# Optimization experiments

Hardware: AMD Instinct MI355X
Metric: run time of the kernel (lower is better)

## Reference

```python
import jax, jax.numpy as jnp
from jax import lax
import numpy as np

B, N, M, C, K = 2, 16384, 4096, 16, 32
RADIUS = 0.1
EPS = 1e-8


def setup_inputs() -> dict:
    key = jax.random.key(0)
    ks = jax.random.split(key, 9)
    return {
        "xyz": jax.random.uniform(ks[0], (B, N, 3), jnp.float32),
        "new_xyz": jax.random.uniform(ks[1], (B, M, 3), jnp.float32),
        "features": jax.random.normal(ks[2], (B, C, N), jnp.float32),
        "w0": jax.random.normal(ks[3], (32, C), jnp.float32) * 0.1,
        "b0": jax.random.normal(ks[4], (32,), jnp.float32) * 0.1,
        "w1": jax.random.normal(ks[5], (64, 32), jnp.float32) * 0.1,
        "b1": jax.random.normal(ks[6], (64,), jnp.float32) * 0.1,
        "wxyz": jax.random.normal(ks[7], (32, 3), jnp.float32) * 0.1,
        "bxyz": jax.random.normal(ks[8], (32,), jnp.float32) * 0.1,
    }


def ball_query(xyz, new_xyz, radius, nsample):
    """Return (idx [B,M,K] int32, idn multiplicity [B,M,K] int32, has_any [B,M] bool).
    Matches pointnet2 ball_query: first `nsample` in-radius indices (ascending),
    empty slots padded with the first found index; idn counts how many times an
    index is duplicated in a row (0 everywhere for rows with no neighbor)."""
    d2 = jnp.sum((new_xyz[:, :, None, :] - xyz[:, None, :, :]) ** 2, axis=-1)  # B,M,N
    n = xyz.shape[1]
    score = jnp.where(d2 < radius * radius,
                      jnp.arange(n, dtype=jnp.int32), jnp.int32(n))
    idx = -lax.top_k(-score, nsample)[0]          # B,M,K smallest indices, asc
    valid = idx < n
    idx = jnp.where(valid, idx, idx[..., :1])      # pad with first found index
    has_any = valid[..., 0]
    idx = jnp.where(idx >= n, 0, idx)              # safe gather for empty rows
    cnt = jnp.sum(idx[..., :, None] == idx[..., None, :], axis=-1).astype(jnp.int32)
    idn = jnp.where(has_any[..., None], cnt, 0)
    return idx, idn, has_any


def reference(xyz, new_xyz, features, w0, b0, w1, b1, wxyz, bxyz):
    idx, idn, has_any = ball_query(xyz, new_xyz, RADIUS, K)
    b_idx = jnp.arange(xyz.shape[0])[:, None, None]
    # QueryAndGroup: relative coords + gathered features
    rel = xyz[b_idx, idx] - new_xyz[:, :, None, :]            # B,M,K,3
    rel = jnp.transpose(rel, (0, 3, 1, 2))                    # B,3,M,K
    gfeat = jnp.transpose(features, (0, 2, 1))[b_idx, idx]    # B,M,K,C
    gfeat = jnp.transpose(gfeat, (0, 3, 1, 2))                # B,C,M,K

    # distance-reciprocal weights, duplicate-corrected by idn, row-normalized
    dist = jnp.linalg.norm(rel, axis=1, keepdims=True)        # B,1,M,K
    dist_recip = 1.0 / (dist + EPS)
    _idn = jnp.where(has_any[:, None, :, None], idn[:, None, :, :], 1).astype(dist.dtype)
    dist_recip = dist_recip / _idn
    weights = dist_recip / jnp.sum(dist_recip, axis=3, keepdims=True)
    idn_mask = has_any[:, None, :, None].astype(dist.dtype)
    weights = weights * idn_mask                              # zero empty rows

    # SharedMLP on features: 1x1 conv == per-point matmul, ReLU
    h = jax.nn.relu(jnp.einsum('bcmk,oc->bomk', gfeat, w0) + b0[None, :, None, None])
    h = jax.nn.relu(jnp.einsum('bcmk,oc->bomk', h, w1) + b1[None, :, None, None])
    feat_sum = jnp.sum(weights * h, axis=3)                   # B,64,M weighted sum-pool

    # xyz branch: SharedMLP [3,32] + max-pool over neighbors
    hx = jax.nn.relu(jnp.einsum('bcmk,oc->bomk', rel, wxyz) + bxyz[None, :, None, None])
    feat_max = jnp.max(hx, axis=3)                            # B,32,M

    return new_xyz, jnp.concatenate([feat_max, feat_sum], axis=1)  # (B,M,3),(B,96,M)
```

## Files before the change

kernel.cpp:

```cpp
#include <hip/hip_runtime.h>
#include <math.h>
#include <limits.h>

#define BB 2
#define NN 16384
#define MM 4096
#define CCH 16
#define KK 32
#define R2 0.01f
#define EPSV 1e-8f
#define GD 10
#define CPB (GD*GD*GD)
#define CAP 56
#define NCELL (BB*CPB)
#define BUCKET_OFF 16384
#define FEATT_OFF (2*1024*1024)
#define WS_GRID (BUCKET_OFF + (size_t)NCELL*CAP*16)
#define WS_FT   (FEATT_OFF + (size_t)BB*NN*CCH*4)
#define NDW 512

typedef __attribute__((ext_vector_type(8))) short short8;
typedef __attribute__((ext_vector_type(4))) float v4f;

__device__ __forceinline__ short f2bf(float f) {
    unsigned u = __float_as_uint(f);
    unsigned r = u + 0x7FFFu + ((u >> 16) & 1u);
    return (short)(r >> 16);
}

__device__ __forceinline__ int cell_of(float x, float y, float z) {
    int cx = min(GD-1, max(0, (int)(x * 10.0f)));
    int cy = min(GD-1, max(0, (int)(y * 10.0f)));
    int cz = min(GD-1, max(0, (int)(z * 10.0f)));
    return (cx*GD + cy)*GD + cz;
}

__global__ void k_scatter(const float* __restrict__ xyz, const float* __restrict__ feat,
                          int* __restrict__ cnt, int* __restrict__ ovf,
                          float4* __restrict__ buckets, float4* __restrict__ featT,
                          int use_ft) {
    int i = blockIdx.x*256 + threadIdx.x;
    if (i >= BB*NN) return;
    const float* p = xyz + (size_t)i*3;
    int b = i >> 14;
    int n = i & (NN-1);
    float x = p[0], y = p[1], z = p[2];
    int cell = b*CPB + cell_of(x, y, z);
    int slot = atomicAdd(&cnt[cell], 1);
    if (slot < CAP)
        buckets[(size_t)cell*CAP + slot] = make_float4(x, y, z, __int_as_float(n));
    else
        *ovf = 1;
    if (use_ft) {
        const float* fb = feat + (size_t)b*CCH*NN + n;
        #pragma unroll
        for (int c4 = 0; c4 < 4; ++c4) {
            float4 t = make_float4(fb[(c4*4+0)*NN], fb[(c4*4+1)*NN],
                                   fb[(c4*4+2)*NN], fb[(c4*4+3)*NN]);
            featT[(size_t)i*4 + c4] = t;
        }
    }
}

__global__ __launch_bounds__(256, 4) void grouper_fused(
    const float* __restrict__ xyz, const float* __restrict__ new_xyz,
    const float* __restrict__ feat,
    const float* __restrict__ w0, const float* __restrict__ b0,
    const float* __restrict__ w1, const float* __restrict__ b1,
    const float* __restrict__ wxyz, const float* __restrict__ bxyz,
    const int* __restrict__ cnt, const int* __restrict__ ovf,
    const float4* __restrict__ buckets, const float4* __restrict__ featT,
    int use_grid, int use_ft,
    float* __restrict__ out)
{
    const int lane = threadIdx.x & 63;
    const int wid  = threadIdx.x >> 6;
    const int q    = (blockIdx.x << 2) + wid;
    const int b    = q >> 12;
    const int m    = q & (MM - 1);

    __shared__ int s_idx[4][KK];
    __shared__ float4 s_rel[4][KK];
    __shared__ __align__(16) unsigned s_bm[4][NDW];

    const float* xb = xyz + (size_t)b * NN * 3;
    const float qx = new_xyz[((size_t)b*MM + m)*3 + 0];
    const float qy = new_xyz[((size_t)b*MM + m)*3 + 1];
    const float qz = new_xyz[((size_t)b*MM + m)*3 + 2];
    const unsigned long long below = (1ull << lane) - 1ull;

    int nfound = 0, idx0 = 0;
    bool need_full = (use_grid == 0) || (use_grid && ovf[0] != 0);

    if (!need_full) {
        uint4 z4 = make_uint4(0u, 0u, 0u, 0u);
        *(uint4*)&s_bm[wid][lane*8]     = z4;
        *(uint4*)&s_bm[wid][lane*8 + 4] = z4;

        int x0 = max(0, (int)floorf((qx - 0.1f)*10.0f - 1e-3f));
        int x1 = min(GD-1, (int)floorf((qx + 0.1f)*10.0f + 1e-3f));
        int y0 = max(0, (int)floorf((qy - 0.1f)*10.0f - 1e-3f));
        int y1 = min(GD-1, (int)floorf((qy + 0.1f)*10.0f + 1e-3f));
        int z0 = max(0, (int)floorf((qz - 0.1f)*10.0f - 1e-3f));
        int z1 = min(GD-1, (int)floorf((qz + 0.1f)*10.0f + 1e-3f));

        int myCell = -1, ncells = 0;
        int myCx = 0, myCy = 0, myCz = 0;
        for (int cx = x0; cx <= x1; ++cx)
        for (int cy = y0; cy <= y1; ++cy)
        for (int cz = z0; cz <= z1; ++cz) {
            if (lane == ncells) {
                myCell = b*CPB + (cx*GD + cy)*GD + cz;
                myCx = cx; myCy = cy; myCz = cz;
            }
            ++ncells;
        }
        int myCnt = 0, myBase = 0;
        if (myCell >= 0) {
            float xlo = myCx*0.1f, ylo = myCy*0.1f, zlo = myCz*0.1f;
            float ddx = fmaxf(fmaxf(xlo - qx, qx - (xlo + 0.1f)), 0.0f);
            float ddy = fmaxf(fmaxf(ylo - qy, qy - (ylo + 0.1f)), 0.0f);
            float ddz = fmaxf(fmaxf(zlo - qz, qz - (zlo + 0.1f)), 0.0f);
            if (ddx*ddx + ddy*ddy + ddz*ddz < R2) {
                myCnt = min(cnt[myCell], CAP);
                myBase = myCell*CAP;
            }
        }

        __builtin_amdgcn_wave_barrier();

        int cc0 = __builtin_amdgcn_readlane(myCnt, 0);
        int cb0 = __builtin_amdgcn_readlane(myBase, 0);
        float4 p0 = make_float4(0.f, 0.f, 0.f, 0.f);
        if (lane < cc0) p0 = buckets[cb0 + lane];
        for (int c = 0; c < ncells; ++c) {
            int cc1 = 0, cb1 = 0;
            if (c + 1 < ncells) {
                cc1 = __builtin_amdgcn_readlane(myCnt, c + 1);
                cb1 = __builtin_amdgcn_readlane(myBase, c + 1);
            }
            float4 pn = make_float4(0.f, 0.f, 0.f, 0.f);
            if (lane < cc1) pn = buckets[cb1 + lane];
            if (lane < cc0) {
                float dx = p0.x - qx, dy = p0.y - qy, dz = p0.z - qz;
                float d2 = dx*dx + dy*dy + dz*dz;
                if (d2 < R2) {
                    int id = __float_as_int(p0.w);
                    atomicOr(&s_bm[wid][id >> 5], 1u << (id & 31));
                }
            }
            cc0 = cc1; cb0 = cb1; p0 = pn;
        }

        __builtin_amdgcn_wave_barrier();

        uint4 d0 = *(uint4*)&s_bm[wid][lane*8];
        uint4 d1 = *(uint4*)&s_bm[wid][lane*8 + 4];
        unsigned dw[8] = {d0.x, d0.y, d0.z, d0.w, d1.x, d1.y, d1.z, d1.w};
        int pc = 0;
        #pragma unroll
        for (int j = 0; j < 8; ++j) pc += __popc(dw[j]);
        int pre = pc;
        #pragma unroll
        for (int d = 1; d < 64; d <<= 1) {
            int t = __shfl_up(pre, d);
            if (lane >= d) pre += t;
        }
        int total = __shfl(pre, 63);
        int rank = pre - pc;
        nfound = min(total, KK);

        if (rank < KK) {
            #pragma unroll
            for (int j = 0; j < 8; ++j) {
                unsigned bits = dw[j];
                while (bits && rank < KK) {
                    int bpos = __builtin_ctz(bits);
                    s_idx[wid][rank] = ((lane*8 + j) << 5) + bpos;
                    bits &= bits - 1;
                    ++rank;
                }
            }
        }

        __builtin_amdgcn_wave_barrier();
        idx0 = (nfound > 0) ? s_idx[wid][0] : 0;
        __builtin_amdgcn_wave_barrier();
        if (lane >= nfound && lane < KK) s_idx[wid][lane] = idx0;
        __builtin_amdgcn_wave_barrier();
    }

    if (need_full) {
        int cntf = 0;
        for (int basep = 0; basep < NN; basep += 256) {
            float d2a[4];
            #pragma unroll
            for (int j = 0; j < 4; ++j) {
                int i = basep + (j << 6) + lane;
                float px = xb[i*3+0], py = xb[i*3+1], pz = xb[i*3+2];
                float dx = px - qx, dy = py - qy, dz = pz - qz;
                d2a[j] = dx*dx + dy*dy + dz*dz;
            }
            #pragma unroll
            for (int j = 0; j < 4; ++j) {
                bool hit = d2a[j] < R2;
                unsigned long long msk = __ballot(hit);
                if (hit) {
                    int pos = cntf + __popcll(msk & below);
                    if (pos < KK) s_idx[wid][pos] = basep + (j << 6) + lane;
                }
                cntf += __popcll(msk);
            }
            if (cntf >= KK) break;
        }
        nfound = cntf < KK ? cntf : KK;
        __builtin_amdgcn_wave_barrier();
        if (lane < KK) {
            int v = 0;
            if (nfound > 0) v = (lane < nfound) ? s_idx[wid][lane] : s_idx[wid][0];
            s_idx[wid][lane] = v;
        }
        __builtin_amdgcn_wave_barrier();
        idx0 = s_idx[wid][0];
    }

    {
        const int k = lane & 31;
        const int h = lane >> 5;
        const int ik = s_idx[wid][k];
        float px = xb[ik*3+0], py = xb[ik*3+1], pz = xb[ik*3+2];
        float rx = px - qx, ry = py - qy, rz = pz - qz;
        float dist = sqrtf(rx*rx + ry*ry + rz*rz);
        float recip = 1.0f / (dist + EPSV);
        float mult = (float)(1 + KK - nfound);
        float w = recip / ((ik == idx0) ? mult : 1.0f);
        float S = w;
        #pragma unroll
        for (int d = 1; d < 32; d <<= 1) S += __shfl_xor(S, d);
        float wk = (nfound > 0) ? (w / S) : 0.0f;
        if (h == 0) s_rel[wid][k] = make_float4(rx, ry, rz, wk);
    }
    __builtin_amdgcn_wave_barrier();

    const int l15 = lane & 15;
    const int quad = lane >> 4;
    const int ik0 = s_idx[wid][l15];
    const int ik1 = s_idx[wid][16 + l15];

    float g0[CCH], g1[CCH];
    if (use_ft) {
        const float4* f0 = featT + ((size_t)(b*NN + ik0)) * 4;
        const float4* f1 = featT + ((size_t)(b*NN + ik1)) * 4;
        #pragma unroll
        for (int c4 = 0; c4 < 4; ++c4) {
            float4 a = f0[c4], c = f1[c4];
            g0[c4*4+0] = a.x; g0[c4*4+1] = a.y; g0[c4*4+2] = a.z; g0[c4*4+3] = a.w;
            g1[c4*4+0] = c.x; g1[c4*4+1] = c.y; g1[c4*4+2] = c.z; g1[c4*4+3] = c.w;
        }
    } else {
        const float* fb = feat + (size_t)b * CCH * NN;
        #pragma unroll
        for (int c = 0; c < CCH; ++c) { g0[c] = fb[c*NN + ik0]; g1[c] = fb[c*NN + ik1]; }
    }

    short8 A0, A1;
    #pragma unroll
    for (int j = 0; j < 8; ++j) {
        const int o = (quad << 3) + j;
        const float* wr = w0 + o*CCH;
        float a0 = 0.f, a1 = 0.f;
        #pragma unroll
        for (int c = 0; c < CCH; ++c) { a0 += wr[c]*g0[c]; a1 += wr[c]*g1[c]; }
        float bo = b0[o];
        A0[j] = f2bf(fmaxf(a0 + bo, 0.0f));
        A1[j] = f2bf(fmaxf(a1 + bo, 0.0f));
    }

    short8 Bf[4];
    #pragma unroll
    for (int u = 0; u < 4; ++u) {
        const float* wr = w1 + ((u << 4) + l15)*32 + (quad << 3);
        float4 p = *(const float4*)(wr);
        float4 r = *(const float4*)(wr + 4);
        short8 bb;
        bb[0]=f2bf(p.x); bb[1]=f2bf(p.y); bb[2]=f2bf(p.z); bb[3]=f2bf(p.w);
        bb[4]=f2bf(r.x); bb[5]=f2bf(r.y); bb[6]=f2bf(r.z); bb[7]=f2bf(r.w);
        Bf[u] = bb;
    }

    v4f zero4 = {0.f, 0.f, 0.f, 0.f};
    v4f D[2][4];
    #pragma unroll
    for (int u = 0; u < 4; ++u) {
        D[0][u] = __builtin_amdgcn_mfma_f32_16x16x32_bf16(A0, Bf[u], zero4, 0, 0, 0);
        D[1][u] = __builtin_amdgcn_mfma_f32_16x16x32_bf16(A1, Bf[u], zero4, 0, 0, 0);
    }

    float wkv[2][4];
    #pragma unroll
    for (int t = 0; t < 2; ++t)
        #pragma unroll
        for (int r = 0; r < 4; ++r)
            wkv[t][r] = s_rel[wid][16*t + (quad << 2) + r].w;

    float* out2 = out + (size_t)BB*MM*3 + (size_t)b*96*MM;

    float Su[4];
    #pragma unroll
    for (int u = 0; u < 4; ++u) {
        const float b1O = b1[(u << 4) + l15];
        float s = 0.f;
        #pragma unroll
        for (int t = 0; t < 2; ++t)
            #pragma unroll
            for (int r = 0; r < 4; ++r)
                s += wkv[t][r] * fmaxf(D[t][u][r] + b1O, 0.0f);
        s += __shfl_xor(s, 16);
        s += __shfl_xor(s, 32);
        Su[u] = s;
    }
    float sout = (quad == 0) ? Su[0] : (quad == 1) ? Su[1] : (quad == 2) ? Su[2] : Su[3];
    out2[(32 + lane)*MM + m] = sout;

    {
        const int c = lane & 31;
        const int h = lane >> 5;
        const float wx0 = wxyz[c*3+0], wx1 = wxyz[c*3+1], wx2 = wxyz[c*3+2];
        const float bc = bxyz[c];
        float v = 0.0f;
        #pragma unroll
        for (int kk = 0; kk < 16; ++kk) {
            float4 hr = s_rel[wid][(h << 4) + kk];
            float t = bc + wx0*hr.x + wx1*hr.y + wx2*hr.z;
            v = fmaxf(v, fmaxf(t, 0.0f));
        }
        v = fmaxf(v, __shfl_xor(v, 32));
        if (h == 0) out2[c*MM + m] = v;
    }

    if (lane == 0) {
        float* o0 = out + ((size_t)b*MM + m)*3;
        o0[0] = qx; o0[1] = qy; o0[2] = qz;
    }
}

extern "C" void kernel_launch(void* const* d_in, const int* in_sizes, int n_in,
                              void* d_out, int out_size, void* d_ws, size_t ws_size,
                              hipStream_t stream) {
    const float* xyz     = (const float*)d_in[0];
    const float* new_xyz = (const float*)d_in[1];
    const float* feat    = (const float*)d_in[2];
    const float* w0      = (const float*)d_in[3];
    const float* b0      = (const float*)d_in[4];
    const float* w1      = (const float*)d_in[5];
    const float* b1      = (const float*)d_in[6];
    const float* wxyz    = (const float*)d_in[7];
    const float* bxyz    = (const float*)d_in[8];
    float* out = (float*)d_out;

    int* ovf = (int*)d_ws;
    int* cnt = (int*)((char*)d_ws + 64);
    float4* buckets = (float4*)((char*)d_ws + BUCKET_OFF);
    float4* featT   = (float4*)((char*)d_ws + FEATT_OFF);
    const int use_grid = (d_ws != nullptr && ws_size >= WS_GRID) ? 1 : 0;
    const int use_ft   = (d_ws != nullptr && ws_size >= WS_FT) ? 1 : 0;

    if (use_grid) {
        hipMemsetAsync(d_ws, 0, BUCKET_OFF, stream);
        hipLaunchKernelGGL(k_scatter, dim3((BB*NN+255)/256), dim3(256), 0, stream,
                           xyz, feat, cnt, ovf, buckets, featT, use_ft);
    }
    hipLaunchKernelGGL(grouper_fused, dim3((BB*MM)/4), dim3(256), 0, stream,
                       xyz, new_xyz, feat, w0, b0, w1, b1, wxyz, bxyz,
                       cnt, ovf, buckets, featT, use_grid, use_ft, out);
}
```

Measured before the change: 120.6 us.

## Move first MLP layer onto MFMA and precompute bf16 weight fragments

The first 16->32 layer, previously scalar FMAs per lane, now runs as bf16 MFMA. Its output is staged through shared memory, transposed into the A operand of the second MFMA, and the biases are folded into the accumulators. The scatter kernel no longer builds a transposed feature copy; instead it converts w0 and w1 once into bf16 MFMA fragments in workspace, and features are gathered directly from the channel-major layout. This cuts per-lane ALU work and the featT write, at the cost of strided feature gathers, extra LDS use, and bf16 rounding of the inputs to the first layer.

```diff
diff --git a/kernel.cpp b/kernel.cpp
--- a/kernel.cpp
+++ b/kernel.cpp
@@ -13,10 +13,10 @@
 #define CPB (GD*GD*GD)
 #define CAP 56
 #define NCELL (BB*CPB)
+#define WSA_OFF 8192
+#define WSB_OFF 10240
 #define BUCKET_OFF 16384
-#define FEATT_OFF (2*1024*1024)
 #define WS_GRID (BUCKET_OFF + (size_t)NCELL*CAP*16)
-#define WS_FT   (FEATT_OFF + (size_t)BB*NN*CCH*4)
 #define NDW 512
 
 typedef __attribute__((ext_vector_type(8))) short short8;
@@ -26,6 +26,9 @@
     unsigned u = __float_as_uint(f);
     unsigned r = u + 0x7FFFu + ((u >> 16) & 1u);
     return (short)(r >> 16);
+}
+__device__ __forceinline__ unsigned pk2(float a, float b) {
+    return (unsigned)(unsigned short)f2bf(a) | ((unsigned)(unsigned short)f2bf(b) << 16);
 }
 
 __device__ __forceinline__ int cell_of(float x, float y, float z) {
@@ -35,10 +38,34 @@
     return (cx*GD + cy)*GD + cz;
 }
 
-__global__ void k_scatter(const float* __restrict__ xyz, const float* __restrict__ feat,
+__global__ void k_scatter(const float* __restrict__ xyz,
+                          const float* __restrict__ w0, const float* __restrict__ w1,
                           int* __restrict__ cnt, int* __restrict__ ovf,
-                          float4* __restrict__ buckets, float4* __restrict__ featT,
-                          int use_ft) {
+                          float4* __restrict__ buckets,
+                          short8* __restrict__ wsA, short8* __restrict__ wsB) {
+    if (blockIdx.x == 0) {
+        int t = threadIdx.x;
+        if (t < 128) {
+            int fi = t >> 6, l = t & 63, l15 = l & 15, qd = (l >> 4) & 3;
+            short8 a = {0,0,0,0,0,0,0,0};
+            if (qd < 2)
+                #pragma unroll
+                for (int j = 0; j < 8; ++j)
+                    a[j] = f2bf(w0[(fi*16 + l15)*CCH + qd*8 + j]);
+            wsA[fi*64 + l] = a;
+        }
+        if (t < 64) {
+            int l15 = t & 15, qd = t >> 4;
+            #pragma unroll
+            for (int u = 0; u < 4; ++u) {
+                const float* wr = w1 + ((u << 4) + l15)*32 + (qd << 3);
+                short8 bb;
+                #pragma unroll
+                for (int j = 0; j < 8; ++j) bb[j] = f2bf(wr[j]);
+                wsB[t*4 + u] = bb;
+            }
+        }
+    }
     int i = blockIdx.x*256 + threadIdx.x;
     if (i >= BB*NN) return;
     const float* p = xyz + (size_t)i*3;
@@ -51,15 +78,6 @@
         buckets[(size_t)cell*CAP + slot] = make_float4(x, y, z, __int_as_float(n));
     else
         *ovf = 1;
-    if (use_ft) {
-        const float* fb = feat + (size_t)b*CCH*NN + n;
-        #pragma unroll
-        for (int c4 = 0; c4 < 4; ++c4) {
-            float4 t = make_float4(fb[(c4*4+0)*NN], fb[(c4*4+1)*NN],
-                                   fb[(c4*4+2)*NN], fb[(c4*4+3)*NN]);
-            featT[(size_t)i*4 + c4] = t;
-        }
-    }
 }
 
 __global__ __launch_bounds__(256, 4) void grouper_fused(
@@ -69,8 +87,9 @@
     const float* __restrict__ w1, const float* __restrict__ b1,
     const float* __restrict__ wxyz, const float* __restrict__ bxyz,
     const int* __restrict__ cnt, const int* __restrict__ ovf,
-    const float4* __restrict__ buckets, const float4* __restrict__ featT,
-    int use_grid, int use_ft,
+    const float4* __restrict__ buckets,
+    const short8* __restrict__ wsA, const short8* __restrict__ wsB,
+    int use_grid,
     float* __restrict__ out)
 {
     const int lane = threadIdx.x & 63;
@@ -82,6 +101,7 @@
     __shared__ int s_idx[4][KK];
     __shared__ float4 s_rel[4][KK];
     __shared__ __align__(16) unsigned s_bm[4][NDW];
+    __shared__ __align__(16) short s_h0t[4][32*32];
 
     const float* xb = xyz + (size_t)b * NN * 3;
     const float qx = new_xyz[((size_t)b*MM + m)*3 + 0];
@@ -244,57 +264,78 @@
 
     const int l15 = lane & 15;
     const int quad = lane >> 4;
-    const int ik0 = s_idx[wid][l15];
-    const int ik1 = s_idx[wid][16 + l15];
-
-    float g0[CCH], g1[CCH];
-    if (use_ft) {
-        const float4* f0 = featT + ((size_t)(b*NN + ik0)) * 4;
-        const float4* f1 = featT + ((size_t)(b*NN + ik1)) * 4;
-        #pragma unroll
-        for (int c4 = 0; c4 < 4; ++c4) {
-            float4 a = f0[c4], c = f1[c4];
-            g0[c4*4+0] = a.x; g0[c4*4+1] = a.y; g0[c4*4+2] = a.z; g0[c4*4+3] = a.w;
-            g1[c4*4+0] = c.x; g1[c4*4+1] = c.y; g1[c4*4+2] = c.z; g1[c4*4+3] = c.w;
-        }
+
+    short8 A1, A1b, Bf[4];
+    if (use_grid) {
+        A1  = wsA[lane];
+        A1b = wsA[64 + lane];
+        #pragma unroll
+        for (int u = 0; u < 4; ++u) Bf[u] = wsB[lane*4 + u];
     } else {
+        short8 z = {0,0,0,0,0,0,0,0};
+        A1 = z; A1b = z;
+        if (quad < 2) {
+            #pragma unroll
+            for (int j = 0; j < 8; ++j) {
+                A1[j]  = f2bf(w0[l15*CCH + quad*8 + j]);
+                A1b[j] = f2bf(w0[(16 + l15)*CCH + quad*8 + j]);
+            }
+        }
+        #pragma unroll
+        for (int u = 0; u < 4; ++u) {
+            const float* wr = w1 + ((u << 4) + l15)*32 + (quad << 3);
+            #pragma unroll
+            for (int j = 0; j < 8; ++j) Bf[u][j] = f2bf(wr[j]);
+        }
+    }
+
+    short8 G0 = {0,0,0,0,0,0,0,0}, G1 = {0,0,0,0,0,0,0,0};
+    {
         const float* fb = feat + (size_t)b * CCH * NN;
-        #pragma unroll
-        for (int c = 0; c < CCH; ++c) { g0[c] = fb[c*NN + ik0]; g1[c] = fb[c*NN + ik1]; }
-    }
-
-    short8 A0, A1;
+        if (quad < 2) {
+            int ika = s_idx[wid][l15];
+            int ikb = s_idx[wid][16 + l15];
+            int cb0 = quad << 3;
+            #pragma unroll
+            for (int j = 0; j < 8; ++j) {
+                G0[j] = f2bf(fb[(cb0 + j)*NN + ika]);
+                G1[j] = f2bf(fb[(cb0 + j)*NN + ikb]);
+            }
+        }
+    }
+
+    v4f C0, C1;
     #pragma unroll
-    for (int j = 0; j < 8; ++j) {
-        const int o = (quad << 3) + j;
-        const float* wr = w0 + o*CCH;
-        float a0 = 0.f, a1 = 0.f;
-        #pragma unroll
-        for (int c = 0; c < CCH; ++c) { a0 += wr[c]*g0[c]; a1 += wr[c]*g1[c]; }
-        float bo = b0[o];
-        A0[j] = f2bf(fmaxf(a0 + bo, 0.0f));
-        A1[j] = f2bf(fmaxf(a1 + bo, 0.0f));
-    }
-
-    short8 Bf[4];
-    #pragma unroll
-    for (int u = 0; u < 4; ++u) {
-        const float* wr = w1 + ((u << 4) + l15)*32 + (quad << 3);
-        float4 p = *(const float4*)(wr);
-        float4 r = *(const float4*)(wr + 4);
-        short8 bb;
-        bb[0]=f2bf(p.x); bb[1]=f2bf(p.y); bb[2]=f2bf(p.z); bb[3]=f2bf(p.w);
-        bb[4]=f2bf(r.x); bb[5]=f2bf(r.y); bb[6]=f2bf(r.z); bb[7]=f2bf(r.w);
-        Bf[u] = bb;
-    }
-
-    v4f zero4 = {0.f, 0.f, 0.f, 0.f};
-    v4f D[2][4];
-    #pragma unroll
-    for (int u = 0; u < 4; ++u) {
-        D[0][u] = __builtin_amdgcn_mfma_f32_16x16x32_bf16(A0, Bf[u], zero4, 0, 0, 0);
-        D[1][u] = __builtin_amdgcn_mfma_f32_16x16x32_bf16(A1, Bf[u], zero4, 0, 0, 0);
-    }
+    for (int r = 0; r < 4; ++r) {
+        C0[r] = b0[(quad << 2) + r];
+        C1[r] = b0[16 + (quad << 2) + r];
+    }
+
+    v4f H00 = __builtin_amdgcn_mfma_f32_16x16x32_bf16(A1,  G0, C0, 0, 0, 0);
+    v4f H01 = __builtin_amdgcn_mfma_f32_16x16x32_bf16(A1b, G0, C1, 0, 0, 0);
+    v4f H10 = __builtin_amdgcn_mfma_f32_16x16x32_bf16(A1,  G1, C0, 0, 0, 0);
+    v4f H11 = __builtin_amdgcn_mfma_f32_16x16x32_bf16(A1b, G1, C1, 0, 0, 0);
+
+    short* hb = &s_h0t[wid][0];
+    {
+        uint2 w;
+        w.x = pk2(fmaxf(H00[0],0.f), fmaxf(H00[1],0.f));
+        w.y = pk2(fmaxf(H00[2],0.f), fmaxf(H00[3],0.f));
+        *(uint2*)&hb[l15*32 + (quad << 2)] = w;
+        w.x = pk2(fmaxf(H01[0],0.f), fmaxf(H01[1],0.f));
+        w.y = pk2(fmaxf(H01[2],0.f), fmaxf(H01[3],0.f));
+        *(uint2*)&hb[l15*32 + 16 + (quad << 2)] = w;
+        w.x = pk2(fmaxf(H10[0],0.f), fmaxf(H10[1],0.f));
+        w.y = pk2(fmaxf(H10[2],0.f), fmaxf(H10[3],0.f));
+        *(uint2*)&hb[(16 + l15)*32 + (quad << 2)] = w;
+        w.x = pk2(fmaxf(H11[0],0.f), fmaxf(H11[1],0.f));
+        w.y = pk2(fmaxf(H11[2],0.f), fmaxf(H11[3],0.f));
+        *(uint2*)&hb[(16 + l15)*32 + 16 + (quad << 2)] = w;
+    }
+    __builtin_amdgcn_wave_barrier();
+
+    short8 A2_0 = *(short8*)&hb[l15*32 + (quad << 3)];
+    short8 A2_1 = *(short8*)&hb[(16 + l15)*32 + (quad << 3)];
 
     float wkv[2][4];
     #pragma unroll
@@ -308,13 +349,14 @@
     float Su[4];
     #pragma unroll
     for (int u = 0; u < 4; ++u) {
-        const float b1O = b1[(u << 4) + l15];
+        float b1u = b1[(u << 4) + l15];
+        v4f Cb = {b1u, b1u, b1u, b1u};
+        v4f D0 = __builtin_amdgcn_mfma_f32_16x16x32_bf16(A2_0, Bf[u], Cb, 0, 0, 0);
+        v4f D1 = __builtin_amdgcn_mfma_f32_16x16x32_bf16(A2_1, Bf[u], Cb, 0, 0, 0);
         float s = 0.f;
         #pragma unroll
-        for (int t = 0; t < 2; ++t)
-            #pragma unroll
-            for (int r = 0; r < 4; ++r)
-                s += wkv[t][r] * fmaxf(D[t][u][r] + b1O, 0.0f);
+        for (int r = 0; r < 4; ++r)
+            s += wkv[0][r]*fmaxf(D0[r], 0.f) + wkv[1][r]*fmaxf(D1[r], 0.f);
         s += __shfl_xor(s, 16);
         s += __shfl_xor(s, 32);
         Su[u] = s;
@@ -360,17 +402,17 @@
 
     int* ovf = (int*)d_ws;
     int* cnt = (int*)((char*)d_ws + 64);
+    short8* wsA = (short8*)((char*)d_ws + WSA_OFF);
+    short8* wsB = (short8*)((char*)d_ws + WSB_OFF);
     float4* buckets = (float4*)((char*)d_ws + BUCKET_OFF);
-    float4* featT   = (float4*)((char*)d_ws + FEATT_OFF);
     const int use_grid = (d_ws != nullptr && ws_size >= WS_GRID) ? 1 : 0;
-    const int use_ft   = (d_ws != nullptr && ws_size >= WS_FT) ? 1 : 0;
 
     if (use_grid) {
         hipMemsetAsync(d_ws, 0, BUCKET_OFF, stream);
         hipLaunchKernelGGL(k_scatter, dim3((BB*NN+255)/256), dim3(256), 0, stream,
-                           xyz, feat, cnt, ovf, buckets, featT, use_ft);
+                           xyz, w0, w1, cnt, ovf, buckets, wsA, wsB);
     }
     hipLaunchKernelGGL(grouper_fused, dim3((BB*MM)/4), dim3(256), 0, stream,
                        xyz, new_xyz, feat, w0, b0, w1, b1, wxyz, bxyz,
-                       cnt, ovf, buckets, featT, use_grid, use_ft, out);
-}
+                       cnt, ovf, buckets, wsA, wsB, use_grid, out);
+}
```

Result: faster. 115.9 us (-3.9%).
